# Optimization experiments

Hardware: AMD Instinct MI355X
Metric: run time of the kernel (lower is better)

## Reference

```python
import jax, jax.numpy as jnp
import numpy as np

N = 67108864  # 2**26, power of 2 as required by the radix-2 Cooley-Tukey recursion


def setup_inputs() -> dict:
    key = jax.random.key(0)
    x = jax.random.normal(key, (N,), dtype=jnp.float32)
    return {"x": x}


def reference(x):
    # The torch module implements the radix-2 Cooley-Tukey recursion, whose
    # mathematical result is exactly the DFT: X[k] = sum_n x[n] exp(-2j*pi*k*n/N).
    # jnp.fft.fft is the clean, efficient, in-place-style equivalent.
    X = jnp.fft.fft(x)
    # Complex output returned as stacked (real, imag) float32 of shape [2, N]
    return jnp.stack([X.real, X.imag]).astype(jnp.float32)
```

## Files before the change

### kernel.cpp

```cpp
#include <hip/hip_runtime.h>

#define PI2F 6.283185307179586476f

__device__ __forceinline__ void dft16(float* xr, float* xi)
{
    const float W16R[16] = {1.f, 1.f, 1.f, 1.f,
                            1.f, 0.92387953251f, 0.70710678119f, 0.38268343236f,
                            1.f, 0.70710678119f, 0.f, -0.70710678119f,
                            1.f, 0.38268343236f, -0.70710678119f, -0.92387953251f};
    const float W16I[16] = {0.f, 0.f, 0.f, 0.f,
                            0.f, -0.38268343236f, -0.70710678119f, -0.92387953251f,
                            0.f, -0.70710678119f, -1.f, -0.70710678119f,
                            0.f, -0.92387953251f, -0.70710678119f, 0.38268343236f};

    float br[16], bi[16];
#pragma unroll
    for (int jl = 0; jl < 4; ++jl) {
        float a0r = xr[jl],      a0i = xi[jl];
        float a1r = xr[jl + 4],  a1i = xi[jl + 4];
        float a2r = xr[jl + 8],  a2i = xi[jl + 8];
        float a3r = xr[jl + 12], a3i = xi[jl + 12];
        float s02r = a0r + a2r, s02i = a0i + a2i;
        float d02r = a0r - a2r, d02i = a0i - a2i;
        float s13r = a1r + a3r, s13i = a1i + a3i;
        float d13r = a1r - a3r, d13i = a1i - a3i;
        br[jl + 0]  = s02r + s13r;  bi[jl + 0]  = s02i + s13i;
        br[jl + 4]  = d02r + d13i;  bi[jl + 4]  = d02i - d13r;
        br[jl + 8]  = s02r - s13r;  bi[jl + 8]  = s02i - s13i;
        br[jl + 12] = d02r - d13i;  bi[jl + 12] = d02i + d13r;
    }
#pragma unroll
    for (int pos = 0; pos < 16; ++pos) {
        float wr = W16R[pos], wi = W16I[pos];
        float tr = br[pos] * wr - bi[pos] * wi;
        bi[pos]  = br[pos] * wi + bi[pos] * wr;
        br[pos]  = tr;
    }
#pragma unroll
    for (int rl = 0; rl < 4; ++rl) {
        float a0r = br[4 * rl + 0], a0i = bi[4 * rl + 0];
        float a1r = br[4 * rl + 1], a1i = bi[4 * rl + 1];
        float a2r = br[4 * rl + 2], a2i = bi[4 * rl + 2];
        float a3r = br[4 * rl + 3], a3i = bi[4 * rl + 3];
        float s02r = a0r + a2r, s02i = a0i + a2i;
        float d02r = a0r - a2r, d02i = a0i - a2i;
        float s13r = a1r + a3r, s13i = a1i + a3i;
        float d13r = a1r - a3r, d13i = a1i - a3i;
        xr[rl + 0]  = s02r + s13r;  xi[rl + 0]  = s02i + s13i;
        xr[rl + 4]  = d02r + d13i;  xi[rl + 4]  = d02i - d13r;
        xr[rl + 8]  = s02r - s13r;  xi[rl + 8]  = s02i - s13i;
        xr[rl + 12] = d02r - d13i;  xi[rl + 12] = d02i + d13r;
    }
}

__global__ __launch_bounds__(256) void fft256_first(const float2* __restrict__ xc,
                                                    float2* __restrict__ yc,
                                                    int Nq,
                                                    float m_inv,
                                                    float m16_inv)
{
    __shared__ __align__(16) float lds[16 * 260 + 4];

    const int tid = threadIdx.x;
    const int f   = tid & 15;
    const int k   = tid >> 4;
    const int t   = blockIdx.x * 16 + f;

    float ar[16], ai[16];
#pragma unroll
    for (int j2 = 0; j2 < 16; ++j2) {
        float2 v = xc[t + (k + 16 * j2) * Nq];
        ar[j2] = v.x;
        ai[j2] = v.y;
    }

    dft16(ar, ai);

    {
        const float mf = (float)(k * Nq + t);
        float ang = -PI2F * (mf * m_inv);
        float w1i, w1r;
        __sincosf(ang, &w1i, &w1r);
        float cw = w1r, sw = w1i;
#pragma unroll
        for (int r1 = 1; r1 < 16; ++r1) {
            float tr = ar[r1] * cw - ai[r1] * sw;
            ai[r1]   = ar[r1] * sw + ai[r1] * cw;
            ar[r1]   = tr;
            float ncw = cw * w1r - sw * w1i;
            sw = cw * w1i + sw * w1r;
            cw = ncw;
        }
    }

    const int wbase = f * 260 + k * 16;
    const int rbase = f * 260 + k;

    float er[16], ei[16];

#pragma unroll
    for (int v = 0; v < 4; ++v)
        *(float4*)&lds[wbase + 4 * v] =
            make_float4(ar[4 * v], ar[4 * v + 1], ar[4 * v + 2], ar[4 * v + 3]);
    __syncthreads();
#pragma unroll
    for (int jj = 0; jj < 16; ++jj)
        er[jj] = lds[rbase + jj * 16];
    __syncthreads();

#pragma unroll
    for (int v = 0; v < 4; ++v)
        *(float4*)&lds[wbase + 4 * v] =
            make_float4(ai[4 * v], ai[4 * v + 1], ai[4 * v + 2], ai[4 * v + 3]);
    __syncthreads();
#pragma unroll
    for (int jj = 0; jj < 16; ++jj)
        ei[jj] = lds[rbase + jj * 16];

    dft16(er, ei);

    {
        float ang2 = -PI2F * ((float)t * m16_inv);
        float u1i, u1r;
        __sincosf(ang2, &u1i, &u1r);
        float cw = u1r, sw = u1i;
#pragma unroll
        for (int r2 = 1; r2 < 16; ++r2) {
            float tr = er[r2] * cw - ei[r2] * sw;
            ei[r2]   = er[r2] * sw + ei[r2] * cw;
            er[r2]   = tr;
            float ncw = cw * u1r - sw * u1i;
            sw = cw * u1i + sw * u1r;
            cw = ncw;
        }
    }

    float2* img = (float2*)lds;
    __syncthreads();
#pragma unroll
    for (int b = 0; b < 2; ++b) {
        if ((f >> 3) == b) {
            const int fr = f & 7;
#pragma unroll
            for (int r2 = 0; r2 < 16; ++r2)
                img[fr * 258 + k + 16 * r2] = make_float2(er[r2], ei[r2]);
        }
        __syncthreads();
        const int base = (blockIdx.x * 16 + 8 * b) * 256;
#pragma unroll
        for (int i = 0; i < 8; ++i)
            yc[base + i * 256 + tid] = img[i * 258 + tid];
        if (b == 0) __syncthreads();
    }
}

__global__ __launch_bounds__(512) void fft256_mid(const float2* __restrict__ xc,
                                                  float2* __restrict__ yc,
                                                  int Nq,
                                                  int sl,
                                                  float n_inv,
                                                  float n16_inv)
{
    __shared__ float lds[32 * 257 + 4];

    const int tid = threadIdx.x;
    const int f   = tid & 31;
    const int k   = tid >> 5;
    const int t   = blockIdx.x * 32 + f;
    const int s   = 1 << sl;
    const int q   = t & (s - 1);
    const int p   = t >> sl;

    float ar[16], ai[16];
#pragma unroll
    for (int j2 = 0; j2 < 16; ++j2) {
        float2 v = xc[t + (k + 16 * j2) * Nq];
        ar[j2] = v.x;
        ai[j2] = v.y;
    }

    dft16(ar, ai);

    {
        const int   m  = k * (Nq >> sl) + p;
        float ang = -PI2F * ((float)m * n_inv);
        float w1i, w1r;
        __sincosf(ang, &w1i, &w1r);
        float cw = w1r, sw = w1i;
#pragma unroll
        for (int r1 = 1; r1 < 16; ++r1) {
            float tr = ar[r1] * cw - ai[r1] * sw;
            ai[r1]   = ar[r1] * sw + ai[r1] * cw;
            ar[r1]   = tr;
            float ncw = cw * w1r - sw * w1i;
            sw = cw * w1i + sw * w1r;
            cw = ncw;
        }
    }

    const int wbase = f * 257 + k * 16;
    const int rbase = f * 257 + k;

    float er[16], ei[16];

#pragma unroll
    for (int r1 = 0; r1 < 16; ++r1)
        lds[wbase + r1] = ar[r1];
    __syncthreads();
#pragma unroll
    for (int jj = 0; jj < 16; ++jj)
        er[jj] = lds[rbase + jj * 16];
    __syncthreads();

#pragma unroll
    for (int r1 = 0; r1 < 16; ++r1)
        lds[wbase + r1] = ai[r1];
    __syncthreads();
#pragma unroll
    for (int jj = 0; jj < 16; ++jj)
        ei[jj] = lds[rbase + jj * 16];

    dft16(er, ei);

    const int dstbase = q + ((256 * p + k) << sl);
    float ang2 = -PI2F * ((float)p * n16_inv);
    float u1i, u1r;
    __sincosf(ang2, &u1i, &u1r);

    yc[dstbase] = make_float2(er[0], ei[0]);
    float cw = u1r, sw = u1i;
#pragma unroll
    for (int r2 = 1; r2 < 16; ++r2) {
        int dst = dstbase + ((16 * r2) << sl);
        yc[dst] = make_float2(er[r2] * cw - ei[r2] * sw,
                              er[r2] * sw + ei[r2] * cw);
        float ncw = cw * u1r - sw * u1i;
        sw = cw * u1i + sw * u1r;
        cw = ncw;
    }
}

__global__ __launch_bounds__(256) void rfft_final(const float2* __restrict__ Zp,
                                                  float* __restrict__ xre,
                                                  float* __restrict__ xim,
                                                  int K,
                                                  float w_scale)
{
    const int k = blockIdx.x * 256 + threadIdx.x;
    const int half = K >> 1;
    if (k > half) return;
    const int M = K << 1;

    if (k == 0) {
        float2 A = Zp[0], B = Zp[K];
        float z0r = A.x + B.x, z0i = A.y + B.y;
        float zkr = A.x - B.x, zki = A.y - B.y;
        xre[0]     = z0r + z0i;  xim[0]     = 0.f;
        xre[M]     = z0r - z0i;  xim[M]     = 0.f;
        xre[K]     = zkr;        xim[K]     = -zki;
        xre[M + K] = zkr;        xim[M + K] = zki;
        return;
    }

    float2 A = Zp[k], B = Zp[k + K], C = Zp[K - k], D = Zp[M - k];

    float Z1r = A.x + B.x, Z1i = A.y + B.y;
    float Zmr = C.x - D.x, Zmi = C.y - D.y;
    float Y1r = C.x + D.x, Y1i = C.y + D.y;
    float Ymr = A.x - B.x, Ymi = A.y - B.y;

    float ang = w_scale * (float)k;
    float Wi, Wr;
    __sincosf(ang, &Wi, &Wr);

    {
        float Er = 0.5f * (Z1r + Zmr), Ei = 0.5f * (Z1i - Zmi);
        float Or = 0.5f * (Z1i + Zmi), Oi = 0.5f * (Zmr - Z1r);
        float WOr = Wr * Or - Wi * Oi, WOi = Wr * Oi + Wi * Or;
        float xr1 = Er + WOr, xi1 = Ei + WOi;
        float xr2 = Er - WOr, xi2 = Ei - WOi;
        xre[k]         = xr1;  xim[k]         = xi1;
        xre[k + M]     = xr2;  xim[k + M]     = xi2;
        xre[M - k]     = xr2;  xim[M - k]     = -xi2;
        xre[2 * M - k] = xr1;  xim[2 * M - k] = -xi1;
    }
    {
        float Wpr = -Wi, Wpi = -Wr;
        float Er = 0.5f * (Y1r + Ymr), Ei = 0.5f * (Y1i - Ymi);
        float Or = 0.5f * (Y1i + Ymi), Oi = 0.5f * (Ymr - Y1r);
        float WOr = Wpr * Or - Wpi * Oi, WOi = Wpr * Oi + Wpi * Or;
        float xr1 = Er + WOr, xi1 = Ei + WOi;
        float xr2 = Er - WOr, xi2 = Ei - WOi;
        xre[K - k]         = xr1;  xim[K - k]         = xi1;
        xre[K - k + M]     = xr2;  xim[K - k + M]     = xi2;
        xre[K + k]         = xr2;  xim[K + k]         = -xi2;
        xre[M + K + k]     = xr1;  xim[M + K + k]     = -xi1;
    }
}

__global__ __launch_bounds__(256) void fft4_first(const float* __restrict__ x,
                                                  float* __restrict__ yre,
                                                  float* __restrict__ yim,
                                                  int Nq, float n_inv)
{
    int p = blockIdx.x * 256 + threadIdx.x;
    if (p >= Nq) return;

    float a = x[p];
    float b = x[p + Nq];
    float c = x[p + 2 * Nq];
    float d = x[p + 3 * Nq];

    float apc = a + c, amc = a - c;
    float bpd = b + d, bmd = b - d;

    float ang = -PI2F * ((float)p * n_inv);
    float w1i, w1r;
    __sincosf(ang, &w1i, &w1r);
    float w2r = w1r * w1r - w1i * w1i, w2i = 2.f * w1r * w1i;
    float w3r = w2r * w1r - w2i * w1i, w3i = w2r * w1i + w2i * w1r;

    float t2 = apc - bpd;
    float4 r4, i4;
    r4.x = apc + bpd;                 i4.x = 0.f;
    r4.y = amc * w1r + bmd * w1i;     i4.y = amc * w1i - bmd * w1r;
    r4.z = t2 * w2r;                  i4.z = t2 * w2i;
    r4.w = amc * w3r - bmd * w3i;     i4.w = amc * w3i + bmd * w3r;

    *(float4*)(yre + 4 * p) = r4;
    *(float4*)(yim + 4 * p) = i4;
}

__global__ __launch_bounds__(256) void fft4_pass(const float* __restrict__ xre,
                                                 const float* __restrict__ xim,
                                                 float* __restrict__ yre,
                                                 float* __restrict__ yim,
                                                 int Nq, int sl, float n_inv)
{
    int t = blockIdx.x * 256 + threadIdx.x;
    if (t >= Nq) return;

    const int s = 1 << sl;
    const int q = t & (s - 1);
    const int p = t >> sl;

    float ar = xre[t],          ai = xim[t];
    float br = xre[t + Nq],     bi = xim[t + Nq];
    float cr = xre[t + 2 * Nq], ci = xim[t + 2 * Nq];
    float dr = xre[t + 3 * Nq], di = xim[t + 3 * Nq];

    float apcr = ar + cr, apci = ai + ci;
    float amcr = ar - cr, amci = ai - ci;
    float bpdr = br + dr, bpdi = bi + di;
    float bmdr = br - dr, bmdi = bi - di;

    float ang = -PI2F * ((float)p * n_inv);
    float w1i, w1r;
    __sincosf(ang, &w1i, &w1r);
    float w2r = w1r * w1r - w1i * w1i, w2i = 2.f * w1r * w1i;
    float w3r = w2r * w1r - w2i * w1i, w3i = w2r * w1i + w2i * w1r;

    const int dst = q + (p << (sl + 2));

    yre[dst] = apcr + bpdr;
    yim[dst] = apci + bpdi;

    float t1r = amcr + bmdi, t1i = amci - bmdr;
    yre[dst + s] = t1r * w1r - t1i * w1i;
    yim[dst + s] = t1r * w1i + t1i * w1r;

    float t2r = apcr - bpdr, t2i = apci - bpdi;
    yre[dst + 2 * s] = t2r * w2r - t2i * w2i;
    yim[dst + 2 * s] = t2r * w2i + t2i * w2r;

    float t3r = amcr - bmdi, t3i = amci + bmdr;
    yre[dst + 3 * s] = t3r * w3r - t3i * w3i;
    yim[dst + 3 * s] = t3r * w3i + t3i * w3r;
}

__global__ __launch_bounds__(256) void bitrev_load(const float* __restrict__ x,
                                                   float* __restrict__ re,
                                                   float* __restrict__ im,
                                                   int N, int logN)
{
    int i = blockIdx.x * 256 + threadIdx.x;
    if (i >= N) return;
    unsigned r = __brev((unsigned)i) >> (32 - logN);
    re[i] = x[r];
    im[i] = 0.f;
}

__global__ __launch_bounds__(256) void r2_stage(float* __restrict__ re,
                                                float* __restrict__ im,
                                                int Nh, int sl, float m_inv)
{
    int t = blockIdx.x * 256 + threadIdx.x;
    if (t >= Nh) return;
    const int half = 1 << sl;
    const int j = t & (half - 1);
    const int pos = ((t >> sl) << (sl + 1)) + j;

    float ang = -PI2F * ((float)j * m_inv);
    float wi, wr;
    __sincosf(ang, &wi, &wr);

    float ur = re[pos],         ui = im[pos];
    float vr0 = re[pos + half], vi0 = im[pos + half];
    float vr = vr0 * wr - vi0 * wi;
    float vi = vr0 * wi + vi0 * wr;

    re[pos] = ur + vr;         im[pos] = ui + vi;
    re[pos + half] = ur - vr;  im[pos + half] = ui - vi;
}


extern "C" void kernel_launch(void* const* d_in, const int* in_sizes, int n_in,
                              void* d_out, int out_size, void* d_ws, size_t ws_size,
                              hipStream_t stream)
{
    const float* x = (const float*)d_in[0];
    const int N = in_sizes[0];
    int logN = 0;
    while ((1 << logN) < N) ++logN;

    float* outre = (float*)d_out;
    float* outim = outre + N;

    if (logN == 26 && ws_size >= (size_t)(N / 2) * sizeof(float2)) {
        const int M  = N >> 1;
        const int K  = M >> 1;
        const int Nq = M >> 8;
        const float fM = (float)M;

        const float2* zc = (const float2*)x;
        float2* wc = (float2*)d_ws;
        float2* oc = (float2*)d_out;

        hipLaunchKernelGGL(fft256_first, dim3(M >> 12), dim3(256), 0, stream,
                           zc, wc, Nq, 1.0f / fM, 16.0f / fM);
        hipLaunchKernelGGL(fft256_mid, dim3(M >> 13), dim3(512), 0, stream,
                           wc, oc, Nq, 8, 256.0f / fM, 4096.0f / fM);
        hipLaunchKernelGGL(fft256_mid, dim3(M >> 13), dim3(512), 0, stream,
                           oc, wc, Nq, 16, 65536.0f / fM, 1048576.0f / fM);
        const int nthreads = (K >> 1) + 1;
        hipLaunchKernelGGL(rfft_final, dim3((nthreads + 255) / 256), dim3(256),
                           0, stream,
                           wc, outre, outim, K, -PI2F / (float)N);
    } else if (((logN & 1) == 0) &&
               ws_size >= (size_t)2 * (size_t)N * sizeof(float)) {
        float* wre = (float*)d_ws;
        float* wim = wre + N;
        const int Nq = N >> 2;
        const int nb = (Nq + 255) / 256;
        hipLaunchKernelGGL(fft4_first, dim3(nb), dim3(256), 0, stream,
                           x, outre, outim, Nq, 1.0f / (float)N);
        float* sre = outre; float* sim = outim;
        float* dre = wre;   float* dim_ = wim;
        const int npass = logN >> 1;
        for (int i = 2; i <= npass; ++i) {
            const int sl = 2 * (i - 1);
            const float n_inv = 1.0f / (float)(N >> sl);
            hipLaunchKernelGGL(fft4_pass, dim3(nb), dim3(256), 0, stream,
                               sre, sim, dre, dim_, Nq, sl, n_inv);
            float* tt;
            tt = sre; sre = dre; dre = tt;
            tt = sim; sim = dim_; dim_ = tt;
        }
    } else {
        const int nbN = (N + 255) / 256;
        hipLaunchKernelGGL(bitrev_load, dim3(nbN), dim3(256), 0, stream,
                           x, outre, outim, N, logN);
        const int Nh = N >> 1;
        const int nbh = (Nh + 255) / 256;
        for (int s = 0; s < logN; ++s) {
            const float m_inv = 1.0f / (float)(2 << s);
            hipLaunchKernelGGL(r2_stage, dim3(nbh), dim3(256), 0, stream,
                               outre, outim, Nh, s, m_inv);
        }
    }
}
```

Measured before the change: 498.8 us.

## Fuse last FFT pass with real-FFT post-processing and add cleanup kernel

Merges the final 256-point FFT pass with the real-to-complex untangling step. Each block computes the two mirrored bins q and -q together, so the Hermitian combine happens in registers. This removes one full write and re-read of the intermediate complex array. A single-block cleanup kernel handles the few boundary bins with a direct 256-point DFT; that kernel is serial and slow per element, and the fused kernel uses more registers and more LDS syncs.

```diff
diff --git a/kernel.cpp b/kernel.cpp
--- a/kernel.cpp
+++ b/kernel.cpp
@@ -240,19 +240,212 @@
     }
 }
 
-__global__ __launch_bounds__(256) void rfft_final(const float2* __restrict__ Zp,
-                                                  float* __restrict__ xre,
-                                                  float* __restrict__ xim,
-                                                  int K,
-                                                  float w_scale)
-{
-    const int k = blockIdx.x * 256 + threadIdx.x;
-    const int half = K >> 1;
-    if (k > half) return;
-    const int M = K << 1;
-
-    if (k == 0) {
-        float2 A = Zp[0], B = Zp[K];
+__global__ __launch_bounds__(512) void fft256_last_fused(
+    const float2* __restrict__ xc,
+    float* __restrict__ xre,
+    float* __restrict__ xim,
+    int Nq,
+    float w_scale)
+{
+    __shared__ float lds[32 * 257 + 4];
+
+    const int tid = threadIdx.x;
+    const int f   = tid & 31;
+    const int k   = tid >> 5;
+    const int i   = f & 15;
+    const int p   = f >> 4;
+    const int b   = blockIdx.x;
+    const int M   = 1 << 25;
+
+    const int qA = 16 * b + i;
+    int qB = 65536 - 16 * b - i;
+    if (qB == 65536) qB = 0;
+
+    float zAr[16], zAi[16];
+
+    {
+        const int t = qA + (p << 16);
+        float ar[16], ai[16];
+#pragma unroll
+        for (int j2 = 0; j2 < 16; ++j2) {
+            float2 v = xc[t + (k + 16 * j2) * Nq];
+            ar[j2] = v.x; ai[j2] = v.y;
+        }
+        dft16(ar, ai);
+        {
+            float ang = -PI2F * ((float)(2 * k + p) * (1.0f / 512.0f));
+            float w1i, w1r; __sincosf(ang, &w1i, &w1r);
+            float cw = w1r, sw = w1i;
+#pragma unroll
+            for (int r1 = 1; r1 < 16; ++r1) {
+                float tr = ar[r1] * cw - ai[r1] * sw;
+                ai[r1]   = ar[r1] * sw + ai[r1] * cw;
+                ar[r1]   = tr;
+                float ncw = cw * w1r - sw * w1i;
+                sw = cw * w1i + sw * w1r; cw = ncw;
+            }
+        }
+        const int wb = f * 257 + k * 16;
+        const int rb = f * 257 + k;
+        float er[16], ei[16];
+#pragma unroll
+        for (int r1 = 0; r1 < 16; ++r1) lds[wb + r1] = ar[r1];
+        __syncthreads();
+#pragma unroll
+        for (int jj = 0; jj < 16; ++jj) er[jj] = lds[rb + jj * 16];
+        __syncthreads();
+#pragma unroll
+        for (int r1 = 0; r1 < 16; ++r1) lds[wb + r1] = ai[r1];
+        __syncthreads();
+#pragma unroll
+        for (int jj = 0; jj < 16; ++jj) ei[jj] = lds[rb + jj * 16];
+        dft16(er, ei);
+        {
+            float ang2 = -PI2F * ((float)p * (1.0f / 32.0f));
+            float u1i, u1r; __sincosf(ang2, &u1i, &u1r);
+            float cw = u1r, sw = u1i;
+#pragma unroll
+            for (int r2 = 1; r2 < 16; ++r2) {
+                float tr = er[r2] * cw - ei[r2] * sw;
+                ei[r2]   = er[r2] * sw + ei[r2] * cw;
+                er[r2]   = tr;
+                float ncw = cw * u1r - sw * u1i;
+                sw = cw * u1i + sw * u1r; cw = ncw;
+            }
+        }
+#pragma unroll
+        for (int r2 = 0; r2 < 16; ++r2) {
+            float orr = __shfl_xor(er[r2], 16);
+            float oii = __shfl_xor(ei[r2], 16);
+            zAr[r2] = p ? (orr - er[r2]) : (er[r2] + orr);
+            zAi[r2] = p ? (oii - ei[r2]) : (ei[r2] + oii);
+        }
+    }
+    __syncthreads();
+
+    {
+        const int t = qB + (p << 16);
+        float ar[16], ai[16];
+#pragma unroll
+        for (int j2 = 0; j2 < 16; ++j2) {
+            float2 v = xc[t + (k + 16 * j2) * Nq];
+            ar[j2] = v.x; ai[j2] = v.y;
+        }
+        dft16(ar, ai);
+        {
+            float ang = -PI2F * ((float)(2 * k + p) * (1.0f / 512.0f));
+            float w1i, w1r; __sincosf(ang, &w1i, &w1r);
+            float cw = w1r, sw = w1i;
+#pragma unroll
+            for (int r1 = 1; r1 < 16; ++r1) {
+                float tr = ar[r1] * cw - ai[r1] * sw;
+                ai[r1]   = ar[r1] * sw + ai[r1] * cw;
+                ar[r1]   = tr;
+                float ncw = cw * w1r - sw * w1i;
+                sw = cw * w1i + sw * w1r; cw = ncw;
+            }
+        }
+        const int wb = f * 257 + k * 16;
+        const int rb = f * 257 + (15 - k);
+        float er[16], ei[16];
+#pragma unroll
+        for (int r1 = 0; r1 < 16; ++r1) lds[wb + r1] = ar[r1];
+        __syncthreads();
+#pragma unroll
+        for (int jj = 0; jj < 16; ++jj) er[jj] = lds[rb + jj * 16];
+        __syncthreads();
+#pragma unroll
+        for (int r1 = 0; r1 < 16; ++r1) lds[wb + r1] = ai[r1];
+        __syncthreads();
+#pragma unroll
+        for (int jj = 0; jj < 16; ++jj) ei[jj] = lds[rb + jj * 16];
+        dft16(er, ei);
+        {
+            float ang2 = -PI2F * ((float)p * (1.0f / 32.0f));
+            float u1i, u1r; __sincosf(ang2, &u1i, &u1r);
+            float cw = u1r, sw = u1i;
+#pragma unroll
+            for (int r2 = 1; r2 < 16; ++r2) {
+                float tr = er[r2] * cw - ei[r2] * sw;
+                ei[r2]   = er[r2] * sw + ei[r2] * cw;
+                er[r2]   = tr;
+                float ncw = cw * u1r - sw * u1i;
+                sw = cw * u1i + sw * u1r; cw = ncw;
+            }
+        }
+
+        const float C15 = 0.0980171403295606f;
+        const float S15 = 0.9951847266721969f;
+        float ang0 = w_scale * (float)(qA + (k << 16));
+        float s0, c0; __sincosf(ang0, &s0, &c0);
+        float Wr = c0 * C15 + s0 * S15;
+        float Wi = s0 * C15 - c0 * S15;
+        if (p) { float tmp = Wr; Wr = Wi; Wi = -tmp; }
+        const bool doW = (qA != 0);
+
+#pragma unroll
+        for (int r2p = 0; r2p < 16; ++r2p) {
+            float orr = __shfl_xor(er[r2p], 16);
+            float oii = __shfl_xor(ei[r2p], 16);
+            float Zmr = p ? (er[r2p] + orr) : (er[r2p] - orr);
+            float Zmi = p ? (ei[r2p] + oii) : (ei[r2p] - oii);
+            if (doW) {
+                const int r2 = 15 - r2p;
+                const int j  = qA + ((k + 16 * r2) << 16) + (p << 24);
+                float Zjr = zAr[r2], Zji = zAi[r2];
+                float Er = 0.5f * (Zjr + Zmr), Ei = 0.5f * (Zji - Zmi);
+                float Or = 0.5f * (Zji + Zmi), Oi = 0.5f * (Zmr - Zjr);
+                float WOr = Wr * Or - Wi * Oi, WOi = Wr * Oi + Wi * Or;
+                float x1r = Er + WOr, x1i = Ei + WOi;
+                float x2r = Er - WOr, x2i = Ei - WOi;
+                xre[j]         = x1r;  xim[j]         = x1i;
+                xre[j + M]     = x2r;  xim[j + M]     = x2i;
+                xre[M - j]     = x2r;  xim[M - j]     = -x2i;
+                xre[2 * M - j] = x1r;  xim[2 * M - j] = -x1i;
+            }
+            float nWr = Wr * S15 - Wi * C15;
+            Wi        = Wr * C15 + Wi * S15;
+            Wr = nWr;
+        }
+    }
+}
+
+__global__ __launch_bounds__(512) void rfft_cleanup(const float2* __restrict__ xc,
+                                                    float* __restrict__ xre,
+                                                    float* __restrict__ xim,
+                                                    int Nq, float w_scale)
+{
+    __shared__ float2 S[1024];
+    const int tid = threadIdx.x;
+
+    for (int out = tid; out < 1024; out += 512) {
+        const int ti = out >> 8, r = out & 255;
+        const int t  = ((ti >> 1) << 15) + ((ti & 1) << 16);
+        float ang = -PI2F * ((float)r * (1.0f / 256.0f));
+        float ws, wc; __sincosf(ang, &ws, &wc);
+        float accr = 0.f, acci = 0.f, cr = 1.f, ci = 0.f;
+        for (int j = 0; j < 256; ++j) {
+            float2 v = xc[t + j * Nq];
+            accr += v.x * cr - v.y * ci;
+            acci += v.x * ci + v.y * cr;
+            float nr = cr * wc - ci * ws;
+            ci = cr * ws + ci * wc; cr = nr;
+        }
+        if (ti & 1) {
+            float ang2 = -PI2F * ((float)r * (1.0f / 512.0f));
+            float s2, c2; __sincosf(ang2, &s2, &c2);
+            float nr = accr * c2 - acci * s2;
+            acci = accr * s2 + acci * c2; accr = nr;
+        }
+        S[(ti << 8) + r] = make_float2(accr, acci);
+    }
+    __syncthreads();
+
+    if (tid >= 257) return;
+    const int K = 1 << 24, M = 1 << 25;
+
+    if (tid == 0) {
+        float2 A = S[0], B = S[256];
         float z0r = A.x + B.x, z0i = A.y + B.y;
         float zkr = A.x - B.x, zki = A.y - B.y;
         xre[0]     = z0r + z0i;  xim[0]     = 0.f;
@@ -262,39 +455,50 @@
         return;
     }
 
-    float2 A = Zp[k], B = Zp[k + K], C = Zp[K - k], D = Zp[M - k];
+    int kk; float2 A, B, C, D;
+    if (tid <= 128) {
+        const int r = tid;
+        kk = r << 16;
+        A = S[r];             B = S[256 + r];
+        C = S[256 - r];       D = S[512 - r];
+    } else {
+        const int r = tid - 129;
+        kk = 32768 + (r << 16);
+        A = S[512 + r];       B = S[768 + r];
+        C = S[512 + 255 - r]; D = S[768 + 255 - r];
+    }
 
     float Z1r = A.x + B.x, Z1i = A.y + B.y;
     float Zmr = C.x - D.x, Zmi = C.y - D.y;
     float Y1r = C.x + D.x, Y1i = C.y + D.y;
     float Ymr = A.x - B.x, Ymi = A.y - B.y;
 
-    float ang = w_scale * (float)k;
-    float Wi, Wr;
-    __sincosf(ang, &Wi, &Wr);
+    float ang = w_scale * (float)kk;
+    float Wi_, Wr_;
+    __sincosf(ang, &Wi_, &Wr_);
 
     {
         float Er = 0.5f * (Z1r + Zmr), Ei = 0.5f * (Z1i - Zmi);
         float Or = 0.5f * (Z1i + Zmi), Oi = 0.5f * (Zmr - Z1r);
-        float WOr = Wr * Or - Wi * Oi, WOi = Wr * Oi + Wi * Or;
+        float WOr = Wr_ * Or - Wi_ * Oi, WOi = Wr_ * Oi + Wi_ * Or;
         float xr1 = Er + WOr, xi1 = Ei + WOi;
         float xr2 = Er - WOr, xi2 = Ei - WOi;
-        xre[k]         = xr1;  xim[k]         = xi1;
-        xre[k + M]     = xr2;  xim[k + M]     = xi2;
-        xre[M - k]     = xr2;  xim[M - k]     = -xi2;
-        xre[2 * M - k] = xr1;  xim[2 * M - k] = -xi1;
+        xre[kk]         = xr1;  xim[kk]         = xi1;
+        xre[kk + M]     = xr2;  xim[kk + M]     = xi2;
+        xre[M - kk]     = xr2;  xim[M - kk]     = -xi2;
+        xre[2 * M - kk] = xr1;  xim[2 * M - kk] = -xi1;
     }
     {
-        float Wpr = -Wi, Wpi = -Wr;
+        float Wpr = -Wi_, Wpi = -Wr_;
         float Er = 0.5f * (Y1r + Ymr), Ei = 0.5f * (Y1i - Ymi);
         float Or = 0.5f * (Y1i + Ymi), Oi = 0.5f * (Ymr - Y1r);
         float WOr = Wpr * Or - Wpi * Oi, WOi = Wpr * Oi + Wpi * Or;
         float xr1 = Er + WOr, xi1 = Ei + WOi;
         float xr2 = Er - WOr, xi2 = Ei - WOi;
-        xre[K - k]         = xr1;  xim[K - k]         = xi1;
-        xre[K - k + M]     = xr2;  xim[K - k + M]     = xi2;
-        xre[K + k]         = xr2;  xim[K + k]         = -xi2;
-        xre[M + K + k]     = xr1;  xim[M + K + k]     = -xi1;
+        xre[K - kk]         = xr1;  xim[K - kk]         = xi1;
+        xre[K - kk + M]     = xr2;  xim[K - kk + M]     = xi2;
+        xre[K + kk]         = xr2;  xim[K + kk]         = -xi2;
+        xre[M + K + kk]     = xr1;  xim[M + K + kk]     = -xi1;
     }
 }
 
@@ -428,24 +632,22 @@
 
     if (logN == 26 && ws_size >= (size_t)(N / 2) * sizeof(float2)) {
         const int M  = N >> 1;
-        const int K  = M >> 1;
         const int Nq = M >> 8;
         const float fM = (float)M;
+        const float wsc = -PI2F / (float)N;
 
         const float2* zc = (const float2*)x;
         float2* wc = (float2*)d_ws;
         float2* oc = (float2*)d_out;
 
         hipLaunchKernelGGL(fft256_first, dim3(M >> 12), dim3(256), 0, stream,
-                           zc, wc, Nq, 1.0f / fM, 16.0f / fM);
+                           zc, oc, Nq, 1.0f / fM, 16.0f / fM);
         hipLaunchKernelGGL(fft256_mid, dim3(M >> 13), dim3(512), 0, stream,
-                           wc, oc, Nq, 8, 256.0f / fM, 4096.0f / fM);
-        hipLaunchKernelGGL(fft256_mid, dim3(M >> 13), dim3(512), 0, stream,
-                           oc, wc, Nq, 16, 65536.0f / fM, 1048576.0f / fM);
-        const int nthreads = (K >> 1) + 1;
-        hipLaunchKernelGGL(rfft_final, dim3((nthreads + 255) / 256), dim3(256),
-                           0, stream,
-                           wc, outre, outim, K, -PI2F / (float)N);
+                           oc, wc, Nq, 8, 256.0f / fM, 4096.0f / fM);
+        hipLaunchKernelGGL(fft256_last_fused, dim3(M >> 14), dim3(512), 0,
+                           stream, wc, outre, outim, Nq, wsc);
+        hipLaunchKernelGGL(rfft_cleanup, dim3(1), dim3(512), 0, stream,
+                           wc, outre, outim, Nq, wsc);
     } else if (((logN & 1) == 0) &&
                ws_size >= (size_t)2 * (size_t)N * sizeof(float)) {
         float* wre = (float*)d_ws;
```

Result: slower. 805.6 us (+61.5%).
